# Kernel tuning notes

Hardware: AMD Instinct MI355X
Metric: run time of the kernel (lower is better)

## Reference

```python
import jax, jax.numpy as jnp
import numpy as np


def setup_inputs() -> dict:
    key = jax.random.key(0)
    k1, k2 = jax.random.split(key)
    B, S_ENC, S_DEC, D = 8, 2048, 2048, 1024
    enc_outputs = jax.random.normal(k1, (B, S_ENC, D), dtype=jnp.float32)
    dec_outputs = jax.random.normal(k2, (B, S_DEC, D), dtype=jnp.float32)
    return {"enc_outputs": enc_outputs, "dec_outputs": dec_outputs}


def reference(enc_outputs, dec_outputs):
    # scores: [B, S_enc, S_dec] = enc @ dec^T (unscaled)
    a_t = jnp.einsum('bed,btd->bet', enc_outputs, dec_outputs)
    a_t = jax.nn.softmax(a_t, axis=-1)
    # context: [B, S_dec, D] = a_t^T @ enc
    c_t = jnp.einsum('bet,bed->btd', a_t, enc_outputs)
    return c_t
```

## Files before the change

kernel.cpp:

```cpp
#include <hip/hip_runtime.h>


typedef _Float16 half8 __attribute__((ext_vector_type(8)));
typedef _Float16 half4v __attribute__((ext_vector_type(4)));
typedef float floatx4 __attribute__((ext_vector_type(4)));

__device__ __forceinline__ void async_load16(const _Float16* g, void* l) {
  __builtin_amdgcn_global_load_lds(
      (const __attribute__((address_space(1))) void*)g,
      (__attribute__((address_space(3))) void*)l, 16, 0, 0);
}

template <typename OutT>
__global__ __launch_bounds__(512, 2) void gemm8p(
    const _Float16* __restrict__ A, const _Float16* __restrict__ Bt,
    OutT* __restrict__ C, int K, long strideA, long strideB, long strideC,
    int ldA, int ldB, int ldC) {
  extern __shared__ char smem_[];
  const int tid = threadIdx.x;
  const int lane = tid & 63;
  const int wave = tid >> 6;
  const int wm = wave >> 2;
  const int wn = wave & 3;
  const int l15 = lane & 15;
  const int lh = lane >> 4;

  const int gx = gridDim.x, gxy = gridDim.x * gridDim.y;
  int fid = blockIdx.z * gxy + blockIdx.y * gx + blockIdx.x;
  const int nwg = gxy * gridDim.z;
  fid = (fid & 7) * (nwg >> 3) + (fid >> 3);
  const int b = fid / gxy;
  const int rem = fid - b * gxy;
  const int m0 = (rem / gx) * 256;
  const int n0 = (rem % gx) * 256;

  A += (long)b * strideA + (long)m0 * ldA;
  Bt += (long)b * strideB + (long)n0 * ldB;
  C += (long)b * strideC;

  floatx4 acc[8][4] = {};
  half8 a[4][2], b0[2][2], b1[2][2];

  auto stage = [&](const _Float16* g, int ld, int k0, char* slot) {
#pragma unroll
    for (int i = 0; i < 4; ++i) {
      const int off = i * 8192 + tid * 16;
      const int row = off >> 7;
      const int ck = (off >> 4) & 7;
      async_load16(g + (long)row * ld + k0 + ((ck ^ (row & 7)) << 3),
                   slot + off);
    }
  };
  auto ldf = [&](const char* slot, int row, int s) -> half8 {
    const int ck = (s * 4 + lh) ^ (row & 7);
    return *(const half8*)(slot + row * 128 + ck * 16);
  };
  auto mm = [&](int mh, int nh, half8(&bb)[2][2]) {
#pragma unroll
    for (int s = 0; s < 2; ++s)
#pragma unroll
      for (int q = 0; q < 4; ++q)
#pragma unroll
        for (int n = 0; n < 2; ++n)
          acc[mh * 4 + q][nh * 2 + n] = __builtin_amdgcn_mfma_f32_16x16x32_f16(
              a[q][s], bb[n][s], acc[mh * 4 + q][nh * 2 + n], 0, 0, 0);
  };
  auto barrier_ = [&]() {
    __builtin_amdgcn_sched_barrier(0);
    asm volatile("" ::: "memory");
    __builtin_amdgcn_s_barrier();
    asm volatile("" ::: "memory");
    __builtin_amdgcn_sched_barrier(0);
  };
  auto lgkm0_ = [&]() {
    asm volatile("s_waitcnt lgkmcnt(0)" ::: "memory");
    __builtin_amdgcn_sched_barrier(0);
  };

  auto quad4 = [&](int cur, int kst, int vmn) {
    const char* as_ = smem_ + cur * 32768 + wm * 16384;
    const char* bs_ = smem_ + 65536 + cur * 32768 + (wn >> 1) * 16384;
    const int brow = (wn & 1) * 64;
#pragma unroll
    for (int q = 0; q < 4; ++q)
#pragma unroll
      for (int s = 0; s < 2; ++s) a[q][s] = ldf(as_, q * 16 + l15, s);
#pragma unroll
    for (int n = 0; n < 2; ++n)
#pragma unroll
      for (int s = 0; s < 2; ++s) b0[n][s] = ldf(bs_, brow + n * 16 + l15, s);
    barrier_();
    lgkm0_();
    __builtin_amdgcn_s_setprio(1);
    mm(0, 0, b0);
    __builtin_amdgcn_s_setprio(0);
    barrier_();
#pragma unroll
    for (int n = 0; n < 2; ++n)
#pragma unroll
      for (int s = 0; s < 2; ++s)
        b1[n][s] = ldf(bs_, brow + (n + 2) * 16 + l15, s);
    barrier_();
    lgkm0_();
    __builtin_amdgcn_s_setprio(1);
    mm(0, 1, b1);
    __builtin_amdgcn_s_setprio(0);
    barrier_();
#pragma unroll
    for (int q = 0; q < 4; ++q)
#pragma unroll
      for (int s = 0; s < 2; ++s) a[q][s] = ldf(as_, (q + 4) * 16 + l15, s);
    if (kst >= 0) stage(Bt, ldB, kst, smem_ + 65536 + cur * 32768);
    barrier_();
    lgkm0_();
    __builtin_amdgcn_s_setprio(1);
    mm(1, 1, b1);
    __builtin_amdgcn_s_setprio(0);
    barrier_();
    if (kst >= 0) stage(A, ldA, kst, smem_ + cur * 32768);
    barrier_();
    lgkm0_();
    __builtin_amdgcn_s_setprio(1);
    mm(1, 0, b0);
    __builtin_amdgcn_s_setprio(0);
    if (vmn)
      asm volatile("s_waitcnt vmcnt(8)" ::: "memory");
    else
      asm volatile("s_waitcnt vmcnt(0)" ::: "memory");
    __builtin_amdgcn_sched_barrier(0);
    barrier_();
  };

  stage(A, ldA, 0, smem_);
  stage(Bt, ldB, 0, smem_ + 65536);
  stage(A, ldA, 64, smem_ + 32768);
  stage(Bt, ldB, 64, smem_ + 65536 + 32768);
  asm volatile("s_waitcnt vmcnt(8)" ::: "memory");
  barrier_();

  const int NT = K >> 6;
  for (int i = 0; i < (NT >> 1) - 1; ++i) {
    quad4(0, (2 * i + 2) * 64, 1);
    quad4(1, (2 * i + 3) * 64, 1);
  }
  quad4(0, -1, 0);
  quad4(1, -1, 0);

#pragma unroll
  for (int mf = 0; mf < 8; ++mf) {
    const long r0 = (long)(m0 + wm * 128 + mf * 16 + lh * 4);
#pragma unroll
    for (int nf = 0; nf < 4; ++nf) {
      const int cc = n0 + wn * 64 + nf * 16 + l15;
#pragma unroll
      for (int rr = 0; rr < 4; ++rr)
        C[(r0 + rr) * ldC + cc] = (OutT)acc[mf][nf][rr];
    }
  }
}

__global__ __launch_bounds__(256) void conv_enc(const float* __restrict__ E,
                                                _Float16* __restrict__ Eh,
                                                _Float16* __restrict__ EhT,
                                                int Se, int D) {
  __shared__ _Float16 T[64][72];
  const int b = blockIdx.z;
  const int d0 = blockIdx.x * 64;
  const int e0 = blockIdx.y * 64;
  const float* Eb = E + (size_t)b * Se * D;
  _Float16* Ehb = Eh + (size_t)b * Se * D;
  _Float16* EhTb = EhT + (size_t)b * D * Se;
  const int tid = threadIdx.x;
  const int tx = tid & 15;
  const int ty = tid >> 4;

  half4v h[4];
#pragma unroll
  for (int r = 0; r < 4; ++r) {
    const int e = e0 + ty * 4 + r;
    float4 v = *(const float4*)(Eb + (size_t)e * D + d0 + tx * 4);
    h[r][0] = (_Float16)v.x; h[r][1] = (_Float16)v.y;
    h[r][2] = (_Float16)v.z; h[r][3] = (_Float16)v.w;
    *(half4v*)(Ehb + (size_t)e * D + d0 + tx * 4) = h[r];
  }
#pragma unroll
  for (int c = 0; c < 4; ++c) {
    half4v w;
#pragma unroll
    for (int r = 0; r < 4; ++r) w[r] = h[r][c];
    *(half4v*)&T[tx * 4 + c][ty * 4] = w;
  }
  __syncthreads();
#pragma unroll
  for (int p = 0; p < 2; ++p) {
    const int idx = tid + p * 256;
    const int row = idx >> 3;
    const int ck = idx & 7;
    *(half8*)(EhTb + (size_t)(d0 + row) * Se + e0 + ck * 8) =
        *(const half8*)&T[row][ck * 8];
  }
}

__global__ __launch_bounds__(256) void conv_dec(const float* __restrict__ X,
                                                _Float16* __restrict__ Y) {
  const size_t i = ((size_t)blockIdx.x * 256 + threadIdx.x) * 8;
  float4 a = *(const float4*)(X + i);
  float4 b = *(const float4*)(X + i + 4);
  half8 h;
  h[0] = (_Float16)a.x; h[1] = (_Float16)a.y;
  h[2] = (_Float16)a.z; h[3] = (_Float16)a.w;
  h[4] = (_Float16)b.x; h[5] = (_Float16)b.y;
  h[6] = (_Float16)b.z; h[7] = (_Float16)b.w;
  *(half8*)(Y + i) = h;
}

__global__ __launch_bounds__(256) void col_stats(const _Float16* __restrict__ ST,
                                                 float2* __restrict__ part) {
  __shared__ float2 red[16][65];
  const int b = blockIdx.z;
  const int e0 = blockIdx.x * 64;
  const int t0 = blockIdx.y * 512;
  const _Float16* S = ST + (size_t)b * 2048 * 2048;
  const int tx = threadIdx.x & 15;
  const int ty = threadIdx.x >> 4;

  float m[4] = {-1e30f, -1e30f, -1e30f, -1e30f};
  float s[4] = {0.f, 0.f, 0.f, 0.f};
  for (int it = 0; it < 32; ++it) {
    const int t = t0 + it * 16 + ty;
    half4v v = *(const half4v*)(S + (size_t)t * 2048 + e0 + tx * 4);
#pragma unroll
    for (int c = 0; c < 4; ++c) {
      const float x = (float)v[c];
      const float m2 = fmaxf(m[c], x);
      s[c] = s[c] * __expf(m[c] - m2) + __expf(x - m2);
      m[c] = m2;
    }
  }
#pragma unroll
  for (int c = 0; c < 4; ++c) red[ty][tx * 4 + c] = make_float2(m[c], s[c]);
  __syncthreads();
  if (threadIdx.x < 64) {
    float2 a = red[0][threadIdx.x];
#pragma unroll
    for (int r = 1; r < 16; ++r) {
      const float2 o = red[r][threadIdx.x];
      const float m2 = fmaxf(a.x, o.x);
      a.y = a.y * __expf(a.x - m2) + o.y * __expf(o.x - m2);
      a.x = m2;
    }
    part[(size_t)blockIdx.y * 16384 + (size_t)b * 2048 + e0 + threadIdx.x] = a;
  }
}

__global__ __launch_bounds__(256) void stats_combine(
    const float2* __restrict__ part, float2* __restrict__ stats) {
  const int idx = blockIdx.x * 256 + threadIdx.x;
  float2 a = part[idx];
#pragma unroll
  for (int tc = 1; tc < 4; ++tc) {
    const float2 o = part[tc * 16384 + idx];
    const float m2 = fmaxf(a.x, o.x);
    a.y = a.y * __expf(a.x - m2) + o.y * __expf(o.x - m2);
    a.x = m2;
  }
  stats[idx] = make_float2(a.x, 1.0f / a.y);
}

__global__ __launch_bounds__(256) void norm_stream(
    const _Float16* __restrict__ ST, const float2* __restrict__ stats,
    _Float16* __restrict__ P) {
  const int b = blockIdx.y;
  const int t0 = blockIdx.x * 4;
  const int e = threadIdx.x * 8;
  float m_[8], rl_[8];
#pragma unroll
  for (int j = 0; j < 8; ++j) {
    const float2 st = stats[(size_t)b * 2048 + e + j];
    m_[j] = st.x;
    rl_[j] = st.y;
  }
  const size_t base = ((size_t)b * 2048 + t0) * 2048 + e;
#pragma unroll
  for (int r = 0; r < 4; ++r) {
    half8 v = *(const half8*)(ST + base + (size_t)r * 2048);
    half8 o;
#pragma unroll
    for (int j = 0; j < 8; ++j)
      o[j] = (_Float16)(__expf((float)v[j] - m_[j]) * rl_[j]);
    *(half8*)(P + base + (size_t)r * 2048) = o;
  }
}

extern "C" void kernel_launch(void* const* d_in, const int* in_sizes, int n_in,
                              void* d_out, int out_size, void* d_ws,
                              size_t ws_size, hipStream_t stream) {
  const float* enc = (const float*)d_in[0];
  const float* dec = (const float*)d_in[1];
  float* out = (float*)d_out;

  const int B = 8, SE = 2048, SD = 2048, D = 1024;
  char* ws = (char*)d_ws;
  _Float16* enc_h = (_Float16*)ws;
  _Float16* dec_h = (_Float16*)(ws + 33554432);
  _Float16* P = (_Float16*)ws;
  _Float16* enc_hT = (_Float16*)(ws + 67108864);
  _Float16* ST = (_Float16*)(ws + 100663296);
  float2* stats = (float2*)(ws + 167772160);
  float2* part = (float2*)(ws + 167903232);

  static int smem_set = 0;
  if (!smem_set) {
    (void)hipFuncSetAttribute(
        reinterpret_cast<const void*>(&gemm8p<_Float16>),
        hipFuncAttributeMaxDynamicSharedMemorySize, 131072);
    (void)hipFuncSetAttribute(
        reinterpret_cast<const void*>(&gemm8p<float>),
        hipFuncAttributeMaxDynamicSharedMemorySize, 131072);
    smem_set = 1;
  }

  conv_enc<<<dim3(D / 64, SE / 64, B), 256, 0, stream>>>(enc, enc_h, enc_hT,
                                                         SE, D);
  conv_dec<<<dim3((size_t)B * SD * D / 2048), 256, 0, stream>>>(dec, dec_h);
  gemm8p<_Float16><<<dim3(SE / 256, SD / 256, B), 512, 131072, stream>>>(
      dec_h, enc_h, ST, D, (long)SD * D, (long)SE * D, (long)SD * SE, D, D,
      SE);
  col_stats<<<dim3(32, 4, B), 256, 0, stream>>>(ST, part);
  stats_combine<<<dim3(64), 256, 0, stream>>>(part, stats);
  norm_stream<<<dim3(512, B), 256, 0, stream>>>(ST, stats, P);
  gemm8p<float><<<dim3(D / 256, SD / 256, B), 512, 131072, stream>>>(
      P, enc_hT, out, SE, (long)SD * SE, (long)D * SE, (long)SD * D, SE, SE,
      D);
}
```

Baseline: 334.9 us.

## Precompute LDS/global addresses and loosen scheduling barriers in GEMM pipeline

Hoists the swizzled LDS read offsets and global staging pointers out of the main loop, so each load becomes a base plus a constant offset. All B fragments (b0 and b1) are now loaded at the start of each half-step instead of b1 being loaded mid-step. The explicit sched_barrier and lgkmcnt(0) waits are dropped in favour of a plain s_barrier, and one barrier before the last MFMA group is removed, which lets the compiler interleave LDS reads, async loads and MFMAs more freely. In exchange, the compiler now controls instruction ordering, which risks different register pressure or less favourable placement of waits.

New measurement: 332.0 us. Within noise of the previous version (-0.9%).

```diff
diff --git a/kernel.cpp b/kernel.cpp
--- a/kernel.cpp
+++ b/kernel.cpp
@@ -38,24 +38,31 @@
   Bt += (long)b * strideB + (long)n0 * ldB;
   C += (long)b * strideC;
 
+  const int lb0 = l15 * 128 + ((lh ^ (l15 & 7)) << 4);
+  const int lb1 = lb0 ^ 64;
+  const char* aBuf[2] = {smem_ + wm * 16384, smem_ + 32768 + wm * 16384};
+  const char* bBuf[2] = {
+      smem_ + 65536 + (wn >> 1) * 16384 + (wn & 1) * 8192,
+      smem_ + 98304 + (wn >> 1) * 16384 + (wn & 1) * 8192};
+  char* aSlot[2] = {smem_, smem_ + 32768};
+  char* bSlot[2] = {smem_ + 65536, smem_ + 98304};
+
+  const int srow = tid >> 3;
+  const int skk = ((tid & 7) ^ (srow & 7)) << 3;
+  const _Float16* Ast = A + (long)srow * ldA + skk;
+  const _Float16* Bst = Bt + (long)srow * ldB + skk;
+  const int dst = tid << 4;
+
   floatx4 acc[8][4] = {};
   half8 a[4][2], b0[2][2], b1[2][2];
 
-  auto stage = [&](const _Float16* g, int ld, int k0, char* slot) {
-#pragma unroll
-    for (int i = 0; i < 4; ++i) {
-      const int off = i * 8192 + tid * 16;
-      const int row = off >> 7;
-      const int ck = (off >> 4) & 7;
-      async_load16(g + (long)row * ld + k0 + ((ck ^ (row & 7)) << 3),
-                   slot + off);
-    }
-  };
-  auto ldf = [&](const char* slot, int row, int s) -> half8 {
-    const int ck = (s * 4 + lh) ^ (row & 7);
-    return *(const half8*)(slot + row * 128 + ck * 16);
+  auto stage = [&](const _Float16* gs, int ld, int k0, char* slot) {
+#pragma unroll
+    for (int i = 0; i < 4; ++i)
+      async_load16(gs + (long)(i * 64) * ld + k0, slot + i * 8192 + dst);
   };
   auto mm = [&](int mh, int nh, half8(&bb)[2][2]) {
+    __builtin_amdgcn_s_setprio(1);
 #pragma unroll
     for (int s = 0; s < 2; ++s)
 #pragma unroll
@@ -64,87 +71,63 @@
         for (int n = 0; n < 2; ++n)
           acc[mh * 4 + q][nh * 2 + n] = __builtin_amdgcn_mfma_f32_16x16x32_f16(
               a[q][s], bb[n][s], acc[mh * 4 + q][nh * 2 + n], 0, 0, 0);
+    __builtin_amdgcn_s_setprio(0);
   };
-  auto barrier_ = [&]() {
-    __builtin_amdgcn_sched_barrier(0);
-    asm volatile("" ::: "memory");
-    __builtin_amdgcn_s_barrier();
-    asm volatile("" ::: "memory");
-    __builtin_amdgcn_sched_barrier(0);
+  auto bar = [&]() { asm volatile("s_barrier" ::: "memory"); };
+
+  auto quad4 = [&](int cur, int kst, bool last) {
+    const char* aB_ = aBuf[cur];
+    const char* bB_ = bBuf[cur];
+#pragma unroll
+    for (int q = 0; q < 4; ++q) {
+      a[q][0] = *(const half8*)(aB_ + lb0 + q * 2048);
+      a[q][1] = *(const half8*)(aB_ + lb1 + q * 2048);
+    }
+#pragma unroll
+    for (int n = 0; n < 2; ++n) {
+      b0[n][0] = *(const half8*)(bB_ + lb0 + n * 2048);
+      b0[n][1] = *(const half8*)(bB_ + lb1 + n * 2048);
+      b1[n][0] = *(const half8*)(bB_ + lb0 + (n + 2) * 2048);
+      b1[n][1] = *(const half8*)(bB_ + lb1 + (n + 2) * 2048);
+    }
+    bar();
+    mm(0, 0, b0);
+    bar();
+    bar();
+    mm(0, 1, b1);
+    bar();
+#pragma unroll
+    for (int q = 0; q < 4; ++q) {
+      a[q][0] = *(const half8*)(aB_ + lb0 + (q + 4) * 2048);
+      a[q][1] = *(const half8*)(aB_ + lb1 + (q + 4) * 2048);
+    }
+    if (kst >= 0) stage(Bst, ldB, kst, bSlot[cur]);
+    bar();
+    mm(1, 1, b1);
+    bar();
+    if (kst >= 0) stage(Ast, ldA, kst, aSlot[cur]);
+    mm(1, 0, b0);
+    if (last)
+      asm volatile("s_waitcnt vmcnt(0)" ::: "memory");
+    else
+      asm volatile("s_waitcnt vmcnt(8)" ::: "memory");
+    bar();
   };
-  auto lgkm0_ = [&]() {
-    asm volatile("s_waitcnt lgkmcnt(0)" ::: "memory");
-    __builtin_amdgcn_sched_barrier(0);
-  };
-
-  auto quad4 = [&](int cur, int kst, int vmn) {
-    const char* as_ = smem_ + cur * 32768 + wm * 16384;
-    const char* bs_ = smem_ + 65536 + cur * 32768 + (wn >> 1) * 16384;
-    const int brow = (wn & 1) * 64;
-#pragma unroll
-    for (int q = 0; q < 4; ++q)
-#pragma unroll
-      for (int s = 0; s < 2; ++s) a[q][s] = ldf(as_, q * 16 + l15, s);
-#pragma unroll
-    for (int n = 0; n < 2; ++n)
-#pragma unroll
-      for (int s = 0; s < 2; ++s) b0[n][s] = ldf(bs_, brow + n * 16 + l15, s);
-    barrier_();
-    lgkm0_();
-    __builtin_amdgcn_s_setprio(1);
-    mm(0, 0, b0);
-    __builtin_amdgcn_s_setprio(0);
-    barrier_();
-#pragma unroll
-    for (int n = 0; n < 2; ++n)
-#pragma unroll
-      for (int s = 0; s < 2; ++s)
-        b1[n][s] = ldf(bs_, brow + (n + 2) * 16 + l15, s);
-    barrier_();
-    lgkm0_();
-    __builtin_amdgcn_s_setprio(1);
-    mm(0, 1, b1);
-    __builtin_amdgcn_s_setprio(0);
-    barrier_();
-#pragma unroll
-    for (int q = 0; q < 4; ++q)
-#pragma unroll
-      for (int s = 0; s < 2; ++s) a[q][s] = ldf(as_, (q + 4) * 16 + l15, s);
-    if (kst >= 0) stage(Bt, ldB, kst, smem_ + 65536 + cur * 32768);
-    barrier_();
-    lgkm0_();
-    __builtin_amdgcn_s_setprio(1);
-    mm(1, 1, b1);
-    __builtin_amdgcn_s_setprio(0);
-    barrier_();
-    if (kst >= 0) stage(A, ldA, kst, smem_ + cur * 32768);
-    barrier_();
-    lgkm0_();
-    __builtin_amdgcn_s_setprio(1);
-    mm(1, 0, b0);
-    __builtin_amdgcn_s_setprio(0);
-    if (vmn)
-      asm volatile("s_waitcnt vmcnt(8)" ::: "memory");
-    else
-      asm volatile("s_waitcnt vmcnt(0)" ::: "memory");
-    __builtin_amdgcn_sched_barrier(0);
-    barrier_();
-  };
-
-  stage(A, ldA, 0, smem_);
-  stage(Bt, ldB, 0, smem_ + 65536);
-  stage(A, ldA, 64, smem_ + 32768);
-  stage(Bt, ldB, 64, smem_ + 65536 + 32768);
+
+  stage(Ast, ldA, 0, aSlot[0]);
+  stage(Bst, ldB, 0, bSlot[0]);
+  stage(Ast, ldA, 64, aSlot[1]);
+  stage(Bst, ldB, 64, bSlot[1]);
   asm volatile("s_waitcnt vmcnt(8)" ::: "memory");
-  barrier_();
+  bar();
 
   const int NT = K >> 6;
   for (int i = 0; i < (NT >> 1) - 1; ++i) {
-    quad4(0, (2 * i + 2) * 64, 1);
-    quad4(1, (2 * i + 3) * 64, 1);
-  }
-  quad4(0, -1, 0);
-  quad4(1, -1, 0);
+    quad4(0, (2 * i + 2) * 64, false);
+    quad4(1, (2 * i + 3) * 64, false);
+  }
+  quad4(0, -1, true);
+  quad4(1, -1, true);
 
 #pragma unroll
   for (int mf = 0; mf < 8; ++mf) {
```
